# Performance work log

Measured on AMD Instinct MI355X. Metric: run time of the kernel, lower is better.

Reference implementation:

```python
import jax, jax.numpy as jnp
import numpy as np

EPS = 1e-5
NEG_INF = -1e38


def q_shift(x, H, W, gamma=0.25, s=1):
    # x: (B, T, C) with T = H*W. Four channel groups shifted by 1 pixel in +W,-W,+H,-H.
    B, T, C = x.shape
    g = int(C * gamma)
    x4 = x.reshape(B, H, W, C)
    o0 = jnp.pad(x4[..., 0:g], ((0, 0), (0, 0), (s, 0), (0, 0)))[:, :, :W, :]      # shift right along W
    o1 = jnp.pad(x4[..., g:2 * g], ((0, 0), (0, 0), (0, s), (0, 0)))[:, :, s:, :]  # shift left along W
    o2 = jnp.pad(x4[..., 2 * g:3 * g], ((0, 0), (s, 0), (0, 0), (0, 0)))[:, :H, :, :]  # shift down along H
    o3 = jnp.pad(x4[..., 3 * g:4 * g], ((0, 0), (0, s), (0, 0), (0, 0)))[:, s:, :, :]  # shift up along H
    parts = [o0, o1, o2, o3]
    if 4 * g < C:
        parts.append(jnp.zeros((B, H, W, C - 4 * g), x.dtype))
    return jnp.concatenate(parts, axis=-1).reshape(B, T, C)


def wkv(w, u, k, v):
    # Numerically-stable RWKV WKV recurrence.
    # w,u: (C,); k,v: (B,T,C) -> y: (B,T,C)
    B, T, C = k.shape

    def step(carry, kv):
        a, b, p = carry
        kt, vt = kv
        ww = u + kt
        p2 = jnp.maximum(p, ww)
        e1 = jnp.exp(p - p2)
        e2 = jnp.exp(ww - p2)
        y = (e1 * a + e2 * vt) / (e1 * b + e2)
        ww2 = p + w
        p3 = jnp.maximum(ww2, kt)
        f1 = jnp.exp(ww2 - p3)
        f2 = jnp.exp(kt - p3)
        return (f1 * a + f2 * vt, f1 * b + f2, p3), y

    init = (jnp.zeros((B, C), k.dtype), jnp.zeros((B, C), k.dtype),
            jnp.full((B, C), NEG_INF, k.dtype))
    kT = jnp.swapaxes(k, 0, 1)
    vT = jnp.swapaxes(v, 0, 1)
    _, ys = jax.lax.scan(step, init, (kT, vT))
    return jnp.swapaxes(ys, 0, 1)


def layer_norm(x, g, b):
    m = jnp.mean(x, axis=-1, keepdims=True)
    v = jnp.mean(jnp.square(x - m), axis=-1, keepdims=True)
    return (x - m) * jax.lax.rsqrt(v + EPS) * g + b


def setup_inputs() -> dict:
    key = jax.random.key(0)
    ks = jax.random.split(key, 16)
    B, H, W, C = 8, 64, 64, 768
    T = H * W
    sc = 1.0 / np.sqrt(C)
    inp = {
        "x": jax.random.normal(ks[0], (B, T, C), jnp.float32),
        "spatial_decay": jax.random.normal(ks[1], (C,), jnp.float32) * 0.1,
        "spatial_first": jax.random.normal(ks[2], (C,), jnp.float32) * 0.1,
        "mix_k": jax.random.uniform(ks[3], (1, 1, C), jnp.float32),
        "mix_v": jax.random.uniform(ks[4], (1, 1, C), jnp.float32),
        "mix_r": jax.random.uniform(ks[5], (1, 1, C), jnp.float32),
        "Wk": jax.random.normal(ks[6], (C, C), jnp.float32) * sc,
        "Wv": jax.random.normal(ks[7], (C, C), jnp.float32) * sc,
        "Wr": jax.random.normal(ks[8], (C, C), jnp.float32) * sc,
        "Wo": jax.random.normal(ks[9], (C, C), jnp.float32) * sc,
        "ln_g": jnp.ones((C,), jnp.float32),
        "ln_b": jnp.zeros((C,), jnp.float32),
        "Wd1": jax.random.normal(ks[10], (C, C // 4), jnp.float32) * sc,
        "bd1": jnp.zeros((C // 4,), jnp.float32),
        "Wd2": jax.random.normal(ks[11], (C // 4, C), jnp.float32) * (2.0 / np.sqrt(C)),
        "bd2": jnp.full((C,), -3.0, jnp.float32),
        "H": H,
        "W": W,
    }
    return inp


def reference(x, spatial_decay, spatial_first, mix_k, mix_v, mix_r,
              Wk, Wv, Wr, Wo, ln_g, ln_b, Wd1, bd1, Wd2, bd2, H, W):
    B, T, C = x.shape
    xx = q_shift(x, H, W)
    xk = x * mix_k + xx * (1.0 - mix_k)
    xv = x * mix_v + xx * (1.0 - mix_v)
    xr = x * mix_r + xx * (1.0 - mix_r)
    k = xk @ Wk
    v = xv @ Wv
    sr = jax.nn.sigmoid(xr @ Wr)
    # frequency-adaptive decay modulation from global context
    gctx = jnp.mean(x, axis=1)                       # (B, C)
    h = jnp.tanh(gctx @ Wd1 + bd1)                   # (B, C/4)
    mod = jax.nn.sigmoid(h @ Wd2 + bd2)              # (B, C)
    w = spatial_decay + jnp.mean(mod, axis=0)        # (C,)
    y = wkv(w, spatial_first, k, v)                  # (B, T, C)
    y = layer_norm(y, ln_g, ln_b)
    return (sr * y) @ Wo
```

## Files before the change

### kernel.cpp

```cpp
#include <hip/hip_runtime.h>
#include <hip/hip_bf16.h>

typedef __hip_bfloat16 bf16;
typedef short short8 __attribute__((ext_vector_type(8)));
typedef float f32x4 __attribute__((ext_vector_type(4)));

#define T_SEQ 4096
#define HH 64
#define WW2 64
#define C_DIM 768
#define CQ 192
#define LCH 32
#define NCH (T_SEQ / LCH)
#define NCG (C_DIM / 8)
#define TCH 16

__device__ __forceinline__ float b2f(bf16 h) { return __bfloat162float(h); }
__device__ __forceinline__ bf16 f2b(float f) { return __float2bfloat16(f); }
__device__ __forceinline__ float sigmoid_stable(float m) {
  float e = __expf(-fabsf(m));
  return (m >= 0.f) ? 1.f / (1.f + e) : e / (1.f + e);
}

union V16 { uint4 u; bf16 h[8]; };

__global__ void k_detect(const unsigned* __restrict__ p, int* __restrict__ flag) {
  if (threadIdx.x == 0 && blockIdx.x == 0)
    *flag = ((p[0] & 0xFFFFu) == 0u) ? 1 : 0;
}

__global__ void k_convert_b(const void* __restrict__ src, bf16* __restrict__ dst,
                            int n, const int* __restrict__ flag) {
  int i = blockIdx.x * blockDim.x + threadIdx.x;
  if (i >= n) return;
  dst[i] = (*flag) ? f2b(((const float*)src)[i]) : ((const bf16*)src)[i];
}

__global__ void k_convert_small(
    const void* s0, const void* s1, const void* s2, const void* s3, const void* s4,
    const void* s5, const void* s6, const void* s7, const void* s8,
    float* d0, float* d1, float* d2, float* d3, float* d4,
    float* d5, float* d6, float* d7, float* d8, const int* __restrict__ flag) {
  const void* srcs[9] = {s0, s1, s2, s3, s4, s5, s6, s7, s8};
  float* dsts[9] = {d0, d1, d2, d3, d4, d5, d6, d7, d8};
  int a = blockIdx.x;
  int n = (a == 8) ? CQ : C_DIM;
  const void* s = srcs[a];
  float* d = dsts[a];
  bool f32 = (*flag != 0);
  for (int i = threadIdx.x; i < n; i += 256)
    d[i] = f32 ? ((const float*)s)[i] : b2f(((const bf16*)s)[i]);
}

__global__ void k_transpose_d(const void* __restrict__ src, bf16* __restrict__ dst,
                              const int* __restrict__ flag) {
  __shared__ bf16 tile[32][33];
  bool f32 = (*flag != 0);
  int bx = blockIdx.x * 32, by = blockIdx.y * 32;
  int tx = threadIdx.x, ty = threadIdx.y;
  for (int j = ty; j < 32; j += 8) {
    size_t idx = (size_t)(by + j) * C_DIM + bx + tx;
    tile[j][tx] = f32 ? f2b(((const float*)src)[idx]) : ((const bf16*)src)[idx];
  }
  __syncthreads();
  for (int j = ty; j < 32; j += 8)
    dst[(size_t)(bx + j) * C_DIM + by + tx] = tile[tx][j];
}

__global__ void k_shift_mix1(const void* __restrict__ xsrc,
                             const float* __restrict__ mix,
                             bf16* __restrict__ dst, int BT,
                             const int* __restrict__ flag) {
  int idx = blockIdx.x * blockDim.x + threadIdx.x;
  if (idx >= BT * (C_DIM / 8)) return;
  bool f32 = (*flag != 0);
  int c8 = (idx % (C_DIM / 8)) * 8;
  int tg = idx / (C_DIM / 8);
  int t = tg & (T_SEQ - 1);
  int hh = t >> 6, ww = t & (WW2 - 1);
  int g = c8 / CQ;
  int d; bool valid;
  if (g == 0)      { valid = (ww >= 1);        d = -1;   }
  else if (g == 1) { valid = (ww <= WW2 - 2);  d = 1;    }
  else if (g == 2) { valid = (hh >= 1);        d = -WW2; }
  else             { valid = (hh <= HH - 2);   d = WW2;  }
  ptrdiff_t base = (ptrdiff_t)tg * C_DIM + c8;
  float fx[8], fxx[8];
  if (f32) {
    const float* xp = (const float*)xsrc;
#pragma unroll
    for (int i = 0; i < 8; i++) fx[i] = xp[base + i];
    if (valid) {
#pragma unroll
      for (int i = 0; i < 8; i++) fxx[i] = xp[base + (ptrdiff_t)d * C_DIM + i];
    } else {
#pragma unroll
      for (int i = 0; i < 8; i++) fxx[i] = 0.f;
    }
  } else {
    const bf16* xp = (const bf16*)xsrc;
    V16 xin; xin.u = *(const uint4*)(xp + base);
    V16 xxv;
    if (valid) xxv.u = *(const uint4*)(xp + base + (ptrdiff_t)d * C_DIM);
    else       xxv.u = make_uint4(0u, 0u, 0u, 0u);
#pragma unroll
    for (int i = 0; i < 8; i++) { fx[i] = b2f(xin.h[i]); fxx[i] = b2f(xxv.h[i]); }
  }
  V16 o;
#pragma unroll
  for (int i = 0; i < 8; i++)
    o.h[i] = f2b(fxx[i] + mix[c8 + i] * (fx[i] - fxx[i]));
  *(uint4*)(dst + base) = o.u;
}

__global__ __launch_bounds__(256) void k_shift_mix3(
    const void* __restrict__ xsrc,
    const float* __restrict__ mk, const float* __restrict__ mv, const float* __restrict__ mr,
    bf16* __restrict__ xk, bf16* __restrict__ xv, bf16* __restrict__ xr,
    float* __restrict__ gpart, const int* __restrict__ flag) {
  __shared__ float sh[C_DIM];
  int tid = threadIdx.x;
  sh[tid] = 0.f; sh[tid + 256] = 0.f; sh[tid + 512] = 0.f;
  __syncthreads();
  int gid = blockIdx.x * 256 + tid;
  bool f32 = (*flag != 0);
  int cg = gid % NCG;
  int tc = gid / NCG;
  int c0 = cg * 8;
  int b = tc / (T_SEQ / TCH);
  int t0 = (tc % (T_SEQ / TCH)) * TCH;
  int g = c0 / CQ;
  float mkv[8], mvv[8], mrv[8];
#pragma unroll
  for (int i = 0; i < 8; i++) { mkv[i] = mk[c0 + i]; mvv[i] = mv[c0 + i]; mrv[i] = mr[c0 + i]; }
  float gs[8];
#pragma unroll
  for (int i = 0; i < 8; i++) gs[i] = 0.f;
  for (int tt = 0; tt < TCH; tt++) {
    int t = t0 + tt;
    int hh = t >> 6, ww = t & (WW2 - 1);
    int d; bool valid;
    if (g == 0)      { valid = (ww >= 1);        d = -1;   }
    else if (g == 1) { valid = (ww <= WW2 - 2);  d = 1;    }
    else if (g == 2) { valid = (hh >= 1);        d = -WW2; }
    else             { valid = (hh <= HH - 2);   d = WW2;  }
    ptrdiff_t base = ((ptrdiff_t)b * T_SEQ + t) * C_DIM + c0;
    float fx[8], fxx[8];
    if (f32) {
      const float* xp = (const float*)xsrc;
      float4 a0 = *(const float4*)(xp + base);
      float4 a1 = *(const float4*)(xp + base + 4);
      fx[0] = a0.x; fx[1] = a0.y; fx[2] = a0.z; fx[3] = a0.w;
      fx[4] = a1.x; fx[5] = a1.y; fx[6] = a1.z; fx[7] = a1.w;
      if (valid) {
        float4 b0 = *(const float4*)(xp + base + (ptrdiff_t)d * C_DIM);
        float4 b1 = *(const float4*)(xp + base + (ptrdiff_t)d * C_DIM + 4);
        fxx[0] = b0.x; fxx[1] = b0.y; fxx[2] = b0.z; fxx[3] = b0.w;
        fxx[4] = b1.x; fxx[5] = b1.y; fxx[6] = b1.z; fxx[7] = b1.w;
      } else {
#pragma unroll
        for (int i = 0; i < 8; i++) fxx[i] = 0.f;
      }
    } else {
      const bf16* xp = (const bf16*)xsrc;
      V16 xin; xin.u = *(const uint4*)(xp + base);
      V16 xxv;
      if (valid) xxv.u = *(const uint4*)(xp + base + (ptrdiff_t)d * C_DIM);
      else       xxv.u = make_uint4(0u, 0u, 0u, 0u);
#pragma unroll
      for (int i = 0; i < 8; i++) { fx[i] = b2f(xin.h[i]); fxx[i] = b2f(xxv.h[i]); }
    }
    V16 ok, ov, orr;
#pragma unroll
    for (int i = 0; i < 8; i++) {
      gs[i] += fx[i];
      ok.h[i]  = f2b(fxx[i] + mkv[i] * (fx[i] - fxx[i]));
      ov.h[i]  = f2b(fxx[i] + mvv[i] * (fx[i] - fxx[i]));
      orr.h[i] = f2b(fxx[i] + mrv[i] * (fx[i] - fxx[i]));
    }
    *(uint4*)(xk + base) = ok.u;
    *(uint4*)(xv + base) = ov.u;
    *(uint4*)(xr + base) = orr.u;
  }
#pragma unroll
  for (int i = 0; i < 8; i++) atomicAdd(&sh[c0 + i], gs[i]);
  __syncthreads();
  float* gp = gpart + (size_t)blockIdx.x * C_DIM;
  gp[tid] = sh[tid]; gp[tid + 256] = sh[tid + 256]; gp[tid + 512] = sh[tid + 512];
}

__global__ void k_gctx_reduce(const float* __restrict__ gpart, float* __restrict__ gctx,
                              int B, int blk_per_b) {
  int idx = blockIdx.x * 256 + threadIdx.x;
  if (idx >= B * C_DIM) return;
  int b = idx / C_DIM, c = idx % C_DIM;
  const float* pp = gpart + (size_t)b * blk_per_b * C_DIM + c;
  float s = 0.f;
  for (int j = 0; j < blk_per_b; j++) s += pp[(size_t)j * C_DIM];
  gctx[idx] = s;
}

__global__ void k_gctx(const void* __restrict__ xsrc, float* __restrict__ gctx,
                       const int* __restrict__ flag) {
  bool f32 = (*flag != 0);
  int c = threadIdx.x;
  int chunk = blockIdx.x;
  int b = blockIdx.y;
  size_t base = ((size_t)b * T_SEQ + (size_t)chunk * 128) * C_DIM + c;
  float s = 0.f;
  if (f32) {
    const float* p = (const float*)xsrc;
    for (int t = 0; t < 128; t++) s += p[base + (size_t)t * C_DIM];
  } else {
    const bf16* p = (const bf16*)xsrc;
    for (int t = 0; t < 128; t++) s += b2f(p[base + (size_t)t * C_DIM]);
  }
  atomicAdd(&gctx[b * C_DIM + c], s);
}

__global__ void k_mod(const float* __restrict__ gctx,
                      const bf16* __restrict__ Wd1, const float* __restrict__ bd1,
                      const bf16* __restrict__ Wd2, const float* __restrict__ bd2,
                      float* __restrict__ wsum, int B) {
  __shared__ float hsh[CQ];
  int b = blockIdx.x, j = threadIdx.x;
  const float invT = 1.0f / (float)T_SEQ;
  float acc = bd1[j];
  for (int i = 0; i < C_DIM; i++)
    acc += (gctx[b * C_DIM + i] * invT) * b2f(Wd1[(size_t)i * CQ + j]);
  hsh[j] = tanhf(acc);
  __syncthreads();
  float invB = 1.0f / (float)B;
  for (int cc = j; cc < C_DIM; cc += CQ) {
    float m = bd2[cc];
    for (int jj = 0; jj < CQ; jj++)
      m += hsh[jj] * b2f(Wd2[(size_t)jj * C_DIM + cc]);
    atomicAdd(&wsum[cc], sigmoid_stable(m) * invB);
  }
}

__device__ __forceinline__ void g2l16(const void* g, void* s) {
  __builtin_amdgcn_global_load_lds(
      (const __attribute__((address_space(1))) unsigned int*)g,
      (__attribute__((address_space(3))) unsigned int*)s, 16, 0, 0);
}

template <int MODE>
__global__ __launch_bounds__(256) void k_gemm_bt(
    const bf16* __restrict__ A, const bf16* __restrict__ Bt, void* __restrict__ Cout,
    const bf16* __restrict__ Y, const float* __restrict__ stats,
    const float* __restrict__ lng, const float* __restrict__ lnb,
    const int* __restrict__ flag, int nmb) {
  const int K = C_DIM, N = C_DIM;
  const int NNB = C_DIM / 128;
  __shared__ __align__(16) char smem[32768];
  int tid = threadIdx.x;
  int wv = tid >> 6, lane = tid & 63;
  int lm = lane & 15, quad = lane >> 4;

  int nwg = nmb * NNB;
  int orig = blockIdx.x;
  int xcd = orig & 7;
  int q8 = nwg >> 3, r8 = nwg & 7;
  int lin = (xcd < r8) ? (xcd * (q8 + 1) + (orig >> 3))
                       : (r8 * (q8 + 1) + (xcd - r8) * q8 + (orig >> 3));
  int m0 = (lin / NNB) * 128, n0 = (lin % NNB) * 128;
  int wm = (wv & 1) * 64, wn = (wv >> 1) * 64;

  f32x4 acc[4][4];
#pragma unroll
  for (int i = 0; i < 4; i++)
#pragma unroll
    for (int j = 0; j < 4; j++) acc[i][j] = f32x4{0.f, 0.f, 0.f, 0.f};

  const bf16* Abase = A + (size_t)m0 * K;
  const bf16* Bbase = Bt + (size_t)n0 * K;
  int ci0 = wv * 128 + lane;
  int ci1 = wv * 128 + 64 + lane;
  int r0 = ci0 >> 2, r1 = ci1 >> 2;
  size_t off0 = (size_t)r0 * K + (size_t)(((ci0 & 3) ^ (r0 & 3)) * 8);
  size_t off1 = (size_t)r1 * K + (size_t)(((ci1 & 3) ^ (r1 & 3)) * 8);
  char* dstA0 = smem + wv * 2048;
  char* dstA1 = smem + wv * 2048 + 1024;
  char* dstB0 = smem + 16384 + wv * 2048;
  char* dstB1 = smem + 16384 + wv * 2048 + 1024;

  const int NT = K / 32;
  g2l16(Abase + off0, dstA0);
  g2l16(Abase + off1, dstA1);
  g2l16(Bbase + off0, dstB0);
  g2l16(Bbase + off1, dstB1);
  __syncthreads();

  int cur = 0;
  int swz = (lm & 3);
  for (int t = 0; t < NT; ++t) {
    if (t + 1 < NT) {
      int kc = (t + 1) * 32;
      int nb = (cur ^ 1) * 8192;
      g2l16(Abase + off0 + kc, dstA0 + nb);
      g2l16(Abase + off1 + kc, dstA1 + nb);
      g2l16(Bbase + off0 + kc, dstB0 + nb);
      g2l16(Bbase + off1 + kc, dstB1 + nb);
    }
    const bf16* sAr = (const bf16*)(smem + cur * 8192);
    const bf16* sBr = (const bf16*)(smem + 16384 + cur * 8192);
    short8 af[4], bfr[4];
#pragma unroll
    for (int i = 0; i < 4; i++)
      af[i] = *(const short8*)(sAr + (size_t)(wm + i * 16 + lm) * 32 + ((quad ^ swz) * 8));
#pragma unroll
    for (int j = 0; j < 4; j++)
      bfr[j] = *(const short8*)(sBr + (size_t)(wn + j * 16 + lm) * 32 + ((quad ^ swz) * 8));
#pragma unroll
    for (int i = 0; i < 4; i++)
#pragma unroll
      for (int j = 0; j < 4; j++)
        acc[i][j] = __builtin_amdgcn_mfma_f32_16x16x32_bf16(af[i], bfr[j], acc[i][j], 0, 0, 0);
    __syncthreads();
    cur ^= 1;
  }

  bool f32out = (MODE == 2) && (*flag != 0);
  if (!f32out) {
    bf16* sC = (bf16*)smem;
#pragma unroll
    for (int i = 0; i < 4; i++)
#pragma unroll
      for (int j = 0; j < 4; j++)
#pragma unroll
        for (int r = 0; r < 4; r++) {
          int m = wm + i * 16 + quad * 4 + r;
          int n = wn + j * 16 + lm;
          float v = acc[i][j][r];
          if (MODE == 3) v = sigmoid_stable(v);
          sC[m * 128 + n] = f2b(v);
        }
    __syncthreads();
    int c16 = tid & 15, rr0 = tid >> 4;
#pragma unroll
    for (int it = 0; it < 8; it++) {
      int r = rr0 + it * 16;
      V16 val; val.u = *(const uint4*)(sC + r * 128 + c16 * 8);
      size_t gbase = (size_t)(m0 + r) * N + n0 + c16 * 8;
      if (MODE == 3) {
        float mu = stats[2 * (m0 + r)], rs = stats[2 * (m0 + r) + 1];
        V16 yv; yv.u = *(const uint4*)(Y + gbase);
        const float* lg = lng + n0 + c16 * 8;
        const float* lb = lnb + n0 + c16 * 8;
        V16 o;
#pragma unroll
        for (int jj = 0; jj < 8; jj++)
          o.h[jj] = f2b(b2f(val.h[jj]) * ((b2f(yv.h[jj]) - mu) * rs * lg[jj] + lb[jj]));
        *(uint4*)((bf16*)Cout + gbase) = o.u;
      } else {
        *(uint4*)((bf16*)Cout + gbase) = val.u;
      }
    }
  } else {
    float* sCf = (float*)smem;
#pragma unroll
    for (int half = 0; half < 2; half++) {
      if (half) __syncthreads();
      if ((wv & 1) == half) {
#pragma unroll
        for (int i = 0; i < 4; i++)
#pragma unroll
          for (int j = 0; j < 4; j++)
#pragma unroll
            for (int r = 0; r < 4; r++) {
              int mrow = i * 16 + quad * 4 + r;
              int n = wn + j * 16 + lm;
              sCf[mrow * 128 + n] = acc[i][j][r];
            }
      }
      __syncthreads();
      int c32 = tid & 31, rr0 = tid >> 5;
#pragma unroll
      for (int it = 0; it < 8; it++) {
        int r = rr0 + it * 8;
        float4 val = *(const float4*)(sCf + r * 128 + c32 * 4);
        *(float4*)((float*)Cout + (size_t)(m0 + half * 64 + r) * N + n0 + c32 * 4) = val;
      }
    }
  }
}

__device__ __forceinline__ void wkv_acc_step(const V16& kv, const V16& vv,
    const float* __restrict__ w, float* a, float* bb, float* p) {
#pragma unroll
  for (int i = 0; i < 8; i++) {
    float kt = b2f(kv.h[i]), vt = b2f(vv.h[i]);
    float ww2 = p[i] + w[i];
    float p3 = fmaxf(ww2, kt);
    float f1 = __expf(ww2 - p3);
    float f2 = __expf(kt - p3);
    a[i] = f1 * a[i] + f2 * vt;
    bb[i] = f1 * bb[i] + f2;
    p[i] = p3;
  }
}

__device__ __forceinline__ void wkv_out_step(const V16& kv, const V16& vv,
    const float* __restrict__ w, const float* __restrict__ u,
    float* aa, float* bb, float* pp, V16& o) {
#pragma unroll
  for (int i = 0; i < 8; i++) {
    float kt = b2f(kv.h[i]), vt = b2f(vv.h[i]);
    float ww = u[i] + kt;
    float p2 = fmaxf(pp[i], ww);
    float e1 = __expf(pp[i] - p2);
    float e2 = __expf(ww - p2);
    o.h[i] = f2b((e1 * aa[i] + e2 * vt) / (e1 * bb[i] + e2));
    float ww2 = pp[i] + w[i];
    float p3 = fmaxf(ww2, kt);
    float f1 = __expf(ww2 - p3);
    float f2 = __expf(kt - p3);
    aa[i] = f1 * aa[i] + f2 * vt;
    bb[i] = f1 * bb[i] + f2;
    pp[i] = p3;
  }
}

__global__ __launch_bounds__(256) void k_wkv_p1(
    const bf16* __restrict__ kb, const bf16* __restrict__ vb,
    const float* __restrict__ sd, const float* __restrict__ wsum,
    float* __restrict__ ca, float* __restrict__ cb, float* __restrict__ cp, int B) {
  int gid = blockIdx.x * 256 + threadIdx.x;
  if (gid >= B * NCH * NCG) return;
  int cg = gid % NCG;
  int ch = (gid / NCG) % NCH;
  int b  = gid / (NCG * NCH);
  int c0 = cg * 8;
  float w[8], a[8], bbv[8], p[8];
#pragma unroll
  for (int i = 0; i < 8; i++) {
    w[i] = sd[c0 + i] + wsum[c0 + i];
    a[i] = 0.f; bbv[i] = 0.f; p[i] = -1e38f;
  }
  const bf16* kp = kb + ((size_t)b * T_SEQ + (size_t)ch * LCH) * C_DIM + c0;
  const bf16* vp = vb + ((size_t)b * T_SEQ + (size_t)ch * LCH) * C_DIM + c0;
  V16 k0, k1, k2, k3, v0, v1, v2, v3;
  k0.u = *(const uint4*)(kp);              v0.u = *(const uint4*)(vp);
  k1.u = *(const uint4*)(kp + C_DIM);      v1.u = *(const uint4*)(vp + C_DIM);
  k2.u = *(const uint4*)(kp + 2 * C_DIM);  v2.u = *(const uint4*)(vp + 2 * C_DIM);
  k3.u = *(const uint4*)(kp + 3 * C_DIM);  v3.u = *(const uint4*)(vp + 3 * C_DIM);
  for (int t = 0; t + 4 < LCH; t += 4) {
    wkv_acc_step(k0, v0, w, a, bbv, p);
    k0.u = *(const uint4*)(kp + (size_t)(t + 4) * C_DIM); v0.u = *(const uint4*)(vp + (size_t)(t + 4) * C_DIM);
    wkv_acc_step(k1, v1, w, a, bbv, p);
    k1.u = *(const uint4*)(kp + (size_t)(t + 5) * C_DIM); v1.u = *(const uint4*)(vp + (size_t)(t + 5) * C_DIM);
    wkv_acc_step(k2, v2, w, a, bbv, p);
    k2.u = *(const uint4*)(kp + (size_t)(t + 6) * C_DIM); v2.u = *(const uint4*)(vp + (size_t)(t + 6) * C_DIM);
    wkv_acc_step(k3, v3, w, a, bbv, p);
    k3.u = *(const uint4*)(kp + (size_t)(t + 7) * C_DIM); v3.u = *(const uint4*)(vp + (size_t)(t + 7) * C_DIM);
  }
  wkv_acc_step(k0, v0, w, a, bbv, p);
  wkv_acc_step(k1, v1, w, a, bbv, p);
  wkv_acc_step(k2, v2, w, a, bbv, p);
  wkv_acc_step(k3, v3, w, a, bbv, p);
  size_t so = ((size_t)b * NCH + ch) * C_DIM + c0;
#pragma unroll
  for (int i = 0; i < 8; i++) { ca[so + i] = a[i]; cb[so + i] = bbv[i]; cp[so + i] = p[i]; }
}

__global__ void k_wkv_p2(float* __restrict__ ca, float* __restrict__ cb,
                         float* __restrict__ cp,
                         const float* __restrict__ sd, const float* __restrict__ wsum,
                         int B) {
  int tid = blockIdx.x * blockDim.x + threadIdx.x;
  if (tid >= B * C_DIM) return;
  int b = tid / C_DIM, c = tid % C_DIM;
  float wL = (sd[c] + wsum[c]) * (float)LCH;
  float a = 0.f, bb = 0.f, p = -1e38f;
  for (int base = 0; base < NCH; base += 16) {
    float la[16], lb[16], lp[16];
#pragma unroll
    for (int j = 0; j < 16; j++) {
      size_t idx = ((size_t)b * NCH + base + j) * C_DIM + c;
      la[j] = ca[idx]; lb[j] = cb[idx]; lp[j] = cp[idx];
    }
#pragma unroll
    for (int j = 0; j < 16; j++) {
      size_t idx = ((size_t)b * NCH + base + j) * C_DIM + c;
      ca[idx] = a; cb[idx] = bb; cp[idx] = p;
      float pw = p + wL;
      float pn = fmaxf(pw, lp[j]);
      float e1 = __expf(pw - pn);
      float e2 = __expf(lp[j] - pn);
      a = e1 * a + e2 * la[j];
      bb = e1 * bb + e2 * lb[j];
      p = pn;
    }
  }
}

__global__ __launch_bounds__(256) void k_wkv_p3(
    const bf16* __restrict__ kb, const bf16* __restrict__ vb,
    const float* __restrict__ sd, const float* __restrict__ sf,
    const float* __restrict__ wsum,
    const float* __restrict__ ca, const float* __restrict__ cb,
    const float* __restrict__ cp, bf16* __restrict__ y, int B) {
  int gid = blockIdx.x * 256 + threadIdx.x;
  if (gid >= B * NCH * NCG) return;
  int cg = gid % NCG;
  int ch = (gid / NCG) % NCH;
  int b  = gid / (NCG * NCH);
  int c0 = cg * 8;
  size_t so = ((size_t)b * NCH + ch) * C_DIM + c0;
  float w[8], u[8], aa[8], bbv[8], pp[8];
#pragma unroll
  for (int i = 0; i < 8; i++) {
    w[i] = sd[c0 + i] + wsum[c0 + i];
    u[i] = sf[c0 + i];
    aa[i] = ca[so + i]; bbv[i] = cb[so + i]; pp[i] = cp[so + i];
  }
  const bf16* kp = kb + ((size_t)b * T_SEQ + (size_t)ch * LCH) * C_DIM + c0;
  const bf16* vp = vb + ((size_t)b * T_SEQ + (size_t)ch * LCH) * C_DIM + c0;
  bf16* yp = y + ((size_t)b * T_SEQ + (size_t)ch * LCH) * C_DIM + c0;
  V16 k0, k1, k2, k3, v0, v1, v2, v3, o;
  k0.u = *(const uint4*)(kp);              v0.u = *(const uint4*)(vp);
  k1.u = *(const uint4*)(kp + C_DIM);      v1.u = *(const uint4*)(vp + C_DIM);
  k2.u = *(const uint4*)(kp + 2 * C_DIM);  v2.u = *(const uint4*)(vp + 2 * C_DIM);
  k3.u = *(const uint4*)(kp + 3 * C_DIM);  v3.u = *(const uint4*)(vp + 3 * C_DIM);
  for (int t = 0; t + 4 < LCH; t += 4) {
    wkv_out_step(k0, v0, w, u, aa, bbv, pp, o);
    *(uint4*)(yp + (size_t)t * C_DIM) = o.u;
    k0.u = *(const uint4*)(kp + (size_t)(t + 4) * C_DIM); v0.u = *(const uint4*)(vp + (size_t)(t + 4) * C_DIM);
    wkv_out_step(k1, v1, w, u, aa, bbv, pp, o);
    *(uint4*)(yp + (size_t)(t + 1) * C_DIM) = o.u;
    k1.u = *(const uint4*)(kp + (size_t)(t + 5) * C_DIM); v1.u = *(const uint4*)(vp + (size_t)(t + 5) * C_DIM);
    wkv_out_step(k2, v2, w, u, aa, bbv, pp, o);
    *(uint4*)(yp + (size_t)(t + 2) * C_DIM) = o.u;
    k2.u = *(const uint4*)(kp + (size_t)(t + 6) * C_DIM); v2.u = *(const uint4*)(vp + (size_t)(t + 6) * C_DIM);
    wkv_out_step(k3, v3, w, u, aa, bbv, pp, o);
    *(uint4*)(yp + (size_t)(t + 3) * C_DIM) = o.u;
    k3.u = *(const uint4*)(kp + (size_t)(t + 7) * C_DIM); v3.u = *(const uint4*)(vp + (size_t)(t + 7) * C_DIM);
  }
  wkv_out_step(k0, v0, w, u, aa, bbv, pp, o);
  *(uint4*)(yp + (size_t)(LCH - 4) * C_DIM) = o.u;
  wkv_out_step(k1, v1, w, u, aa, bbv, pp, o);
  *(uint4*)(yp + (size_t)(LCH - 3) * C_DIM) = o.u;
  wkv_out_step(k2, v2, w, u, aa, bbv, pp, o);
  *(uint4*)(yp + (size_t)(LCH - 2) * C_DIM) = o.u;
  wkv_out_step(k3, v3, w, u, aa, bbv, pp, o);
  *(uint4*)(yp + (size_t)(LCH - 1) * C_DIM) = o.u;
}

__global__ __launch_bounds__(256) void k_ln_stats(const bf16* __restrict__ y,
                                                  float* __restrict__ stats) {
  int row = blockIdx.x;
  int tid = threadIdx.x;
  const bf16* yr = y + (size_t)row * C_DIM;
  float v0 = b2f(yr[tid]), v1 = b2f(yr[tid + 256]), v2 = b2f(yr[tid + 512]);
  float s1 = v0 + v1 + v2;
  float s2 = v0 * v0 + v1 * v1 + v2 * v2;
#pragma unroll
  for (int off = 32; off >= 1; off >>= 1) {
    s1 += __shfl_xor(s1, off, 64);
    s2 += __shfl_xor(s2, off, 64);
  }
  __shared__ float sh1[4], sh2[4];
  int wv = tid >> 6, lane = tid & 63;
  if (lane == 0) { sh1[wv] = s1; sh2[wv] = s2; }
  __syncthreads();
  if (tid == 0) {
    float t1 = sh1[0] + sh1[1] + sh1[2] + sh1[3];
    float t2 = sh2[0] + sh2[1] + sh2[2] + sh2[3];
    float mean = t1 * (1.f / (float)C_DIM);
    float var = t2 * (1.f / (float)C_DIM) - mean * mean;
    stats[2 * row] = mean;
    stats[2 * row + 1] = rsqrtf(var + 1e-5f);
  }
}

extern "C" void kernel_launch(void* const* d_in, const int* in_sizes, int n_in,
                              void* d_out, int out_size, void* d_ws, size_t ws_size,
                              hipStream_t stream) {
  const void* x   = d_in[0];
  const void* sd  = d_in[1];
  const void* sf  = d_in[2];
  const void* mk  = d_in[3];
  const void* mv  = d_in[4];
  const void* mr  = d_in[5];
  const void* Wk  = d_in[6];
  const void* Wv  = d_in[7];
  const void* Wr  = d_in[8];
  const void* Wo  = d_in[9];
  const void* lng = d_in[10];
  const void* lnb = d_in[11];
  const void* Wd1 = d_in[12];
  const void* bd1 = d_in[13];
  const void* Wd2 = d_in[14];
  const void* bd2 = d_in[15];

  const int C = in_sizes[1];
  const int BT = in_sizes[0] / C;
  const int B = BT / T_SEQ;

  const size_t S  = (size_t)BT * C * sizeof(bf16);
  const size_t WB = (size_t)C * C * sizeof(bf16);
  const size_t WD = (size_t)C * CQ * sizeof(bf16);
  const size_t CS = (size_t)B * NCH * C * sizeof(float);
  const int nblk_mix = (BT / TCH) * NCG / 256;
  const int blk_per_b = nblk_mix / B;
  const size_t GP = (size_t)nblk_mix * C * sizeof(float);
  const size_t rest = 4 * WB + 2 * WD + ((size_t)8 * C + CQ + (size_t)B * C + C) * 4
                      + 16 + 15 + 3 * CS + (size_t)BT * 8 + GP + 256;
  const bool fused = (ws_size >= 3 * S + rest);

  char* p = (char*)d_ws;
  bf16* slot0 = (bf16*)p; p += S;
  bf16* slot1 = (bf16*)p; p += S;
  bf16* slot2 = nullptr;
  if (fused) { slot2 = (bf16*)p; p += S; }
  bf16* WkT = (bf16*)p; p += WB;
  bf16* WvT = (bf16*)p; p += WB;
  bf16* WrT = (bf16*)p; p += WB;
  bf16* WoT = (bf16*)p; p += WB;
  bf16* Wd1c = (bf16*)p; p += WD;
  bf16* Wd2c = (bf16*)p; p += WD;
  float* sd_f  = (float*)p; p += C * 4;
  float* sf_f  = (float*)p; p += C * 4;
  float* mk_f  = (float*)p; p += C * 4;
  float* mv_f  = (float*)p; p += C * 4;
  float* mr_f  = (float*)p; p += C * 4;
  float* lng_f = (float*)p; p += C * 4;
  float* lnb_f = (float*)p; p += C * 4;
  float* bd2_f = (float*)p; p += C * 4;
  float* bd1_f = (float*)p; p += CQ * 4;
  float* gctx  = (float*)p; p += (size_t)B * C * 4;
  float* wsum  = (float*)p; p += C * 4;
  int* flag    = (int*)p; p += 16;
  p = (char*)(((uintptr_t)p + 15) & ~(uintptr_t)15);
  float* ca = (float*)p; p += CS;
  float* cb = (float*)p; p += CS;
  float* cp = (float*)p; p += CS;
  float* stats = (float*)p; p += (size_t)BT * 8;
  float* gpart = (float*)p; p += GP;

  bf16* stage = (bf16*)d_out;

  k_detect<<<1, 64, 0, stream>>>((const unsigned*)lng, flag);
  hipMemsetAsync(gctx, 0, (size_t)(B * C + C) * sizeof(float), stream);

  k_convert_small<<<9, 256, 0, stream>>>(sd, sf, mk, mv, mr, lng, lnb, bd2, bd1,
                                         sd_f, sf_f, mk_f, mv_f, mr_f, lng_f, lnb_f,
                                         bd2_f, bd1_f, flag);
  k_convert_b<<<(C * CQ + 255) / 256, 256, 0, stream>>>(Wd1, Wd1c, C * CQ, flag);
  k_convert_b<<<(C * CQ + 255) / 256, 256, 0, stream>>>(Wd2, Wd2c, C * CQ, flag);

  dim3 tb(32, 8), tg(C / 32, C / 32);
  k_transpose_d<<<tg, tb, 0, stream>>>(Wk, WkT, flag);
  k_transpose_d<<<tg, tb, 0, stream>>>(Wv, WvT, flag);
  k_transpose_d<<<tg, tb, 0, stream>>>(Wr, WrT, flag);
  k_transpose_d<<<tg, tb, 0, stream>>>(Wo, WoT, flag);

  const int nmb = BT / 128;
  const int ngemm = nmb * (C / 128);
  int scan_threads = B * NCH * NCG;
  int scan_blocks = (scan_threads + 255) / 256;

  if (fused) {
    k_shift_mix3<<<nblk_mix, 256, 0, stream>>>(x, mk_f, mv_f, mr_f,
                                               slot0, stage, slot1, gpart, flag);
    k_gctx_reduce<<<(B * C + 255) / 256, 256, 0, stream>>>(gpart, gctx, B, blk_per_b);
    k_mod<<<B, CQ, 0, stream>>>(gctx, Wd1c, bd1_f, Wd2c, bd2_f, wsum, B);

    k_gemm_bt<0><<<ngemm, 256, 0, stream>>>(slot0, WkT, slot2, nullptr, nullptr, nullptr, nullptr, flag, nmb);
    k_gemm_bt<0><<<ngemm, 256, 0, stream>>>(stage, WvT, slot0, nullptr, nullptr, nullptr, nullptr, flag, nmb);

    k_wkv_p1<<<scan_blocks, 256, 0, stream>>>(slot2, slot0, sd_f, wsum, ca, cb, cp, B);
    k_wkv_p2<<<(B * C + 255) / 256, 256, 0, stream>>>(ca, cb, cp, sd_f, wsum, B);
    k_wkv_p3<<<scan_blocks, 256, 0, stream>>>(slot2, slot0, sd_f, sf_f, wsum, ca, cb, cp, stage, B);

    k_ln_stats<<<BT, 256, 0, stream>>>(stage, stats);
    k_gemm_bt<3><<<ngemm, 256, 0, stream>>>(slot1, WrT, slot0, stage, stats, lng_f, lnb_f, flag, nmb);
    k_gemm_bt<2><<<ngemm, 256, 0, stream>>>(slot0, WoT, d_out, nullptr, nullptr, nullptr, nullptr, flag, nmb);
  } else {
    int nthr = BT * (C / 8);
    int nblk = (nthr + 255) / 256;
    k_gctx<<<dim3(32, B), C, 0, stream>>>(x, gctx, flag);
    k_mod<<<B, CQ, 0, stream>>>(gctx, Wd1c, bd1_f, Wd2c, bd2_f, wsum, B);

    k_shift_mix1<<<nblk, 256, 0, stream>>>(x, mk_f, stage, BT, flag);
    k_gemm_bt<0><<<ngemm, 256, 0, stream>>>(stage, WkT, slot0, nullptr, nullptr, nullptr, nullptr, flag, nmb);
    k_shift_mix1<<<nblk, 256, 0, stream>>>(x, mv_f, stage, BT, flag);
    k_gemm_bt<0><<<ngemm, 256, 0, stream>>>(stage, WvT, slot1, nullptr, nullptr, nullptr, nullptr, flag, nmb);

    k_wkv_p1<<<scan_blocks, 256, 0, stream>>>(slot0, slot1, sd_f, wsum, ca, cb, cp, B);
    k_wkv_p2<<<(B * C + 255) / 256, 256, 0, stream>>>(ca, cb, cp, sd_f, wsum, B);
    k_wkv_p3<<<scan_blocks, 256, 0, stream>>>(slot0, slot1, sd_f, sf_f, wsum, ca, cb, cp, stage, B);

    k_ln_stats<<<BT, 256, 0, stream>>>(stage, stats);
    k_shift_mix1<<<nblk, 256, 0, stream>>>(x, mr_f, slot0, BT, flag);
    k_gemm_bt<3><<<ngemm, 256, 0, stream>>>(slot0, WrT, slot1, stage, stats, lng_f, lnb_f, flag, nmb);
    k_gemm_bt<2><<<ngemm, 256, 0, stream>>>(slot1, WoT, d_out, nullptr, nullptr, nullptr, nullptr, flag, nmb);
  }
}
```

Before: 676.3 us.

## Load GEMM operands directly from global memory instead of LDS staging

The GEMM kernel no longer stages A and B tiles through double-buffered LDS with global_load_lds. Each wave now reads its MFMA fragments straight from global memory, relying on the caches, and the K loop is fully unrolled with no barriers. Launch bounds now request 2 blocks per SM. This drops the LDS traffic and the per-step synchronisation. In exchange, the four waves of a block no longer share loaded tiles, so global and L2 traffic rises, and each load is 16-byte strided across rows, which coalesces less well.

```diff
diff --git a/kernel.cpp b/kernel.cpp
--- a/kernel.cpp
+++ b/kernel.cpp
@@ -239,14 +239,8 @@
   }
 }
 
-__device__ __forceinline__ void g2l16(const void* g, void* s) {
-  __builtin_amdgcn_global_load_lds(
-      (const __attribute__((address_space(1))) unsigned int*)g,
-      (__attribute__((address_space(3))) unsigned int*)s, 16, 0, 0);
-}
-
 template <int MODE>
-__global__ __launch_bounds__(256) void k_gemm_bt(
+__global__ __launch_bounds__(256, 2) void k_gemm_rd(
     const bf16* __restrict__ A, const bf16* __restrict__ Bt, void* __restrict__ Cout,
     const bf16* __restrict__ Y, const float* __restrict__ stats,
     const float* __restrict__ lng, const float* __restrict__ lnb,
@@ -273,52 +267,24 @@
 #pragma unroll
     for (int j = 0; j < 4; j++) acc[i][j] = f32x4{0.f, 0.f, 0.f, 0.f};
 
-  const bf16* Abase = A + (size_t)m0 * K;
-  const bf16* Bbase = Bt + (size_t)n0 * K;
-  int ci0 = wv * 128 + lane;
-  int ci1 = wv * 128 + 64 + lane;
-  int r0 = ci0 >> 2, r1 = ci1 >> 2;
-  size_t off0 = (size_t)r0 * K + (size_t)(((ci0 & 3) ^ (r0 & 3)) * 8);
-  size_t off1 = (size_t)r1 * K + (size_t)(((ci1 & 3) ^ (r1 & 3)) * 8);
-  char* dstA0 = smem + wv * 2048;
-  char* dstA1 = smem + wv * 2048 + 1024;
-  char* dstB0 = smem + 16384 + wv * 2048;
-  char* dstB1 = smem + 16384 + wv * 2048 + 1024;
-
-  const int NT = K / 32;
-  g2l16(Abase + off0, dstA0);
-  g2l16(Abase + off1, dstA1);
-  g2l16(Bbase + off0, dstB0);
-  g2l16(Bbase + off1, dstB1);
-  __syncthreads();
-
-  int cur = 0;
-  int swz = (lm & 3);
-  for (int t = 0; t < NT; ++t) {
-    if (t + 1 < NT) {
-      int kc = (t + 1) * 32;
-      int nb = (cur ^ 1) * 8192;
-      g2l16(Abase + off0 + kc, dstA0 + nb);
-      g2l16(Abase + off1 + kc, dstA1 + nb);
-      g2l16(Bbase + off0 + kc, dstB0 + nb);
-      g2l16(Bbase + off1 + kc, dstB1 + nb);
-    }
-    const bf16* sAr = (const bf16*)(smem + cur * 8192);
-    const bf16* sBr = (const bf16*)(smem + 16384 + cur * 8192);
+  const bf16* Aw = A + (size_t)(m0 + wm + lm) * K + quad * 8;
+  const bf16* Bw = Bt + (size_t)(n0 + wn + lm) * K + quad * 8;
+
+#pragma unroll
+  for (int t = 0; t < C_DIM / 32; ++t) {
+    const int kc = t * 32;
     short8 af[4], bfr[4];
 #pragma unroll
     for (int i = 0; i < 4; i++)
-      af[i] = *(const short8*)(sAr + (size_t)(wm + i * 16 + lm) * 32 + ((quad ^ swz) * 8));
+      af[i] = *(const short8*)(Aw + (size_t)i * 16 * K + kc);
 #pragma unroll
     for (int j = 0; j < 4; j++)
-      bfr[j] = *(const short8*)(sBr + (size_t)(wn + j * 16 + lm) * 32 + ((quad ^ swz) * 8));
+      bfr[j] = *(const short8*)(Bw + (size_t)j * 16 * K + kc);
 #pragma unroll
     for (int i = 0; i < 4; i++)
 #pragma unroll
       for (int j = 0; j < 4; j++)
         acc[i][j] = __builtin_amdgcn_mfma_f32_16x16x32_bf16(af[i], bfr[j], acc[i][j], 0, 0, 0);
-    __syncthreads();
-    cur ^= 1;
   }
 
   bool f32out = (MODE == 2) && (*flag != 0);
@@ -667,16 +633,16 @@
     k_gctx_reduce<<<(B * C + 255) / 256, 256, 0, stream>>>(gpart, gctx, B, blk_per_b);
     k_mod<<<B, CQ, 0, stream>>>(gctx, Wd1c, bd1_f, Wd2c, bd2_f, wsum, B);
 
-    k_gemm_bt<0><<<ngemm, 256, 0, stream>>>(slot0, WkT, slot2, nullptr, nullptr, nullptr, nullptr, flag, nmb);
-    k_gemm_bt<0><<<ngemm, 256, 0, stream>>>(stage, WvT, slot0, nullptr, nullptr, nullptr, nullptr, flag, nmb);
+    k_gemm_rd<0><<<ngemm, 256, 0, stream>>>(slot0, WkT, slot2, nullptr, nullptr, nullptr, nullptr, flag, nmb);
+    k_gemm_rd<0><<<ngemm, 256, 0, stream>>>(stage, WvT, slot0, nullptr, nullptr, nullptr, nullptr, flag, nmb);
 
     k_wkv_p1<<<scan_blocks, 256, 0, stream>>>(slot2, slot0, sd_f, wsum, ca, cb, cp, B);
     k_wkv_p2<<<(B * C + 255) / 256, 256, 0, stream>>>(ca, cb, cp, sd_f, wsum, B);
     k_wkv_p3<<<scan_blocks, 256, 0, stream>>>(slot2, slot0, sd_f, sf_f, wsum, ca, cb, cp, stage, B);
 
     k_ln_stats<<<BT, 256, 0, stream>>>(stage, stats);
-    k_gemm_bt<3><<<ngemm, 256, 0, stream>>>(slot1, WrT, slot0, stage, stats, lng_f, lnb_f, flag, nmb);
-    k_gemm_bt<2><<<ngemm, 256, 0, stream>>>(slot0, WoT, d_out, nullptr, nullptr, nullptr, nullptr, flag, nmb);
+    k_gemm_rd<3><<<ngemm, 256, 0, stream>>>(slot1, WrT, slot0, stage, stats, lng_f, lnb_f, flag, nmb);
+    k_gemm_rd<2><<<ngemm, 256, 0, stream>>>(slot0, WoT, d_out, nullptr, nullptr, nullptr, nullptr, flag, nmb);
   } else {
     int nthr = BT * (C / 8);
     int nblk = (nthr + 255) / 256;
@@ -684,9 +650,9 @@
     k_mod<<<B, CQ, 0, stream>>>(gctx, Wd1c, bd1_f, Wd2c, bd2_f, wsum, B);
 
     k_shift_mix1<<<nblk, 256, 0, stream>>>(x, mk_f, stage, BT, flag);
-    k_gemm_bt<0><<<ngemm, 256, 0, stream>>>(stage, WkT, slot0, nullptr, nullptr, nullptr, nullptr, flag, nmb);
+    k_gemm_rd<0><<<ngemm, 256, 0, stream>>>(stage, WkT, slot0, nullptr, nullptr, nullptr, nullptr, flag, nmb);
     k_shift_mix1<<<nblk, 256, 0, stream>>>(x, mv_f, stage, BT, flag);
-    k_gemm_bt<0><<<ngemm, 256, 0, stream>>>(stage, WvT, slot1, nullptr, nullptr, nullptr, nullptr, flag, nmb);
+    k_gemm_rd<0><<<ngemm, 256, 0, stream>>>(stage, WvT, slot1, nullptr, nullptr, nullptr, nullptr, flag, nmb);
 
     k_wkv_p1<<<scan_blocks, 256, 0, stream>>>(slot0, slot1, sd_f, wsum, ca, cb, cp, B);
     k_wkv_p2<<<(B * C + 255) / 256, 256, 0, stream>>>(ca, cb, cp, sd_f, wsum, B);
@@ -694,7 +660,7 @@
 
     k_ln_stats<<<BT, 256, 0, stream>>>(stage, stats);
     k_shift_mix1<<<nblk, 256, 0, stream>>>(x, mr_f, slot0, BT, flag);
-    k_gemm_bt<3><<<ngemm, 256, 0, stream>>>(slot0, WrT, slot1, stage, stats, lng_f, lnb_f, flag, nmb);
-    k_gemm_bt<2><<<ngemm, 256, 0, stream>>>(slot1, WoT, d_out, nullptr, nullptr, nullptr, nullptr, flag, nmb);
-  }
-}
+    k_gemm_rd<3><<<ngemm, 256, 0, stream>>>(slot0, WrT, slot1, stage, stats, lng_f, lnb_f, flag, nmb);
+    k_gemm_rd<2><<<ngemm, 256, 0, stream>>>(slot1, WoT, d_out, nullptr, nullptr, nullptr, nullptr, flag, nmb);
+  }
+}
```

Result: slower. 986.5 us (+45.9%).

## Replace double-buffered K=32 GEMM loop with single-buffered K=64 tiles

Applied to the files above, without the earlier changes.

The GEMM main loop switches from a double-buffered K-step of 32 with prefetch of the next tile to a single-buffered K-step of 64, using a new row/XOR swizzle for the LDS layout. Each iteration now loads the full 64-wide tile, synchronizes, then runs two MFMA sub-steps. This halves the loop trip count and barrier count but removes the overlap between global-to-LDS loads and MFMA compute, so loads are exposed unless other resident waves hide them.

```diff
diff --git a/kernel.cpp b/kernel.cpp
--- a/kernel.cpp
+++ b/kernel.cpp
@@ -275,50 +275,44 @@
 
   const bf16* Abase = A + (size_t)m0 * K;
   const bf16* Bbase = Bt + (size_t)n0 * K;
-  int ci0 = wv * 128 + lane;
-  int ci1 = wv * 128 + 64 + lane;
-  int r0 = ci0 >> 2, r1 = ci1 >> 2;
-  size_t off0 = (size_t)r0 * K + (size_t)(((ci0 & 3) ^ (r0 & 3)) * 8);
-  size_t off1 = (size_t)r1 * K + (size_t)(((ci1 & 3) ^ (r1 & 3)) * 8);
-  char* dstA0 = smem + wv * 2048;
-  char* dstA1 = smem + wv * 2048 + 1024;
-  char* dstB0 = smem + 16384 + wv * 2048;
-  char* dstB1 = smem + 16384 + wv * 2048 + 1024;
-
-  const int NT = K / 32;
-  g2l16(Abase + off0, dstA0);
-  g2l16(Abase + off1, dstA1);
-  g2l16(Bbase + off0, dstB0);
-  g2l16(Bbase + off1, dstB1);
-  __syncthreads();
-
-  int cur = 0;
-  int swz = (lm & 3);
-  for (int t = 0; t < NT; ++t) {
-    if (t + 1 < NT) {
-      int kc = (t + 1) * 32;
-      int nb = (cur ^ 1) * 8192;
-      g2l16(Abase + off0 + kc, dstA0 + nb);
-      g2l16(Abase + off1 + kc, dstA1 + nb);
-      g2l16(Bbase + off0 + kc, dstB0 + nb);
-      g2l16(Bbase + off1 + kc, dstB1 + nb);
-    }
-    const bf16* sAr = (const bf16*)(smem + cur * 8192);
-    const bf16* sBr = (const bf16*)(smem + 16384 + cur * 8192);
-    short8 af[4], bfr[4];
-#pragma unroll
-    for (int i = 0; i < 4; i++)
-      af[i] = *(const short8*)(sAr + (size_t)(wm + i * 16 + lm) * 32 + ((quad ^ swz) * 8));
-#pragma unroll
-    for (int j = 0; j < 4; j++)
-      bfr[j] = *(const short8*)(sBr + (size_t)(wn + j * 16 + lm) * 32 + ((quad ^ swz) * 8));
-#pragma unroll
-    for (int i = 0; i < 4; i++)
+
+  int srw = lane >> 3;
+  int cgs = (lane & 7) ^ ((srw & 1) << 2);
+  size_t offg[4];
+  int dstb[4];
+#pragma unroll
+  for (int s = 0; s < 4; s++) {
+    offg[s] = (size_t)(s * 32 + wv * 8 + srw) * K + (size_t)cgs * 8;
+    dstb[s] = s * 4096 + wv * 1024;
+  }
+
+  const bf16* sA = (const bf16*)smem;
+  const bf16* sB = (const bf16*)(smem + 16384);
+  int rswz = (lm & 1) << 2;
+
+  for (int kc = 0; kc < K; kc += 64) {
+#pragma unroll
+    for (int s = 0; s < 4; s++) {
+      g2l16(Abase + offg[s] + kc, smem + dstb[s]);
+      g2l16(Bbase + offg[s] + kc, smem + 16384 + dstb[s]);
+    }
+    __syncthreads();
+#pragma unroll
+    for (int kk = 0; kk < 2; kk++) {
+      short8 af[4], bfr[4];
+#pragma unroll
+      for (int i = 0; i < 4; i++)
+        af[i] = *(const short8*)(sA + (size_t)(wm + i * 16 + lm) * 64 + (size_t)(((kk << 2) + quad) ^ rswz) * 8);
 #pragma unroll
       for (int j = 0; j < 4; j++)
-        acc[i][j] = __builtin_amdgcn_mfma_f32_16x16x32_bf16(af[i], bfr[j], acc[i][j], 0, 0, 0);
+        bfr[j] = *(const short8*)(sB + (size_t)(wn + j * 16 + lm) * 64 + (size_t)(((kk << 2) + quad) ^ rswz) * 8);
+#pragma unroll
+      for (int i = 0; i < 4; i++)
+#pragma unroll
+        for (int j = 0; j < 4; j++)
+          acc[i][j] = __builtin_amdgcn_mfma_f32_16x16x32_bf16(af[i], bfr[j], acc[i][j], 0, 0, 0);
+    }
     __syncthreads();
-    cur ^= 1;
   }
 
   bool f32out = (MODE == 2) && (*flag != 0);
```

After: 744.4 us. +10.1%, slower.
